# Performance work log

Hardware: AMD Instinct MI355X
Metric: run time of the kernel (lower is better)

## Reference

```python
import jax, jax.numpy as jnp
import numpy as np

N = 100_000       # nodes
E = 1_600_000     # directed edges (avg degree 16)
IN, H, Z = 128, 128, 64


def setup_inputs() -> dict:
    key = jax.random.key(0)
    ks = jax.random.split(key, 8)
    x = jax.random.normal(ks[0], (N, IN), dtype=jnp.float32)
    edge_index = jax.random.randint(ks[1], (2, E), 0, N, dtype=jnp.int32)
    # Glorot-ish init like PyG GCNConv
    W1 = jax.random.normal(ks[2], (IN, H), dtype=jnp.float32) / np.sqrt(IN).astype(np.float32)
    b1 = jnp.zeros((H,), dtype=jnp.float32)
    Wmu = jax.random.normal(ks[3], (H, Z), dtype=jnp.float32) / np.sqrt(H).astype(np.float32)
    bmu = jnp.zeros((Z,), dtype=jnp.float32)
    Wlv = jax.random.normal(ks[4], (H, Z), dtype=jnp.float32) / np.sqrt(H).astype(np.float32)
    blv = jnp.zeros((Z,), dtype=jnp.float32)
    return {"x": x, "edge_index": edge_index, "W1": W1, "b1": b1,
            "Wmu": Wmu, "bmu": bmu, "Wlv": Wlv, "blv": blv}


def _gcn_conv(x, src, dst, norm, W, b):
    """PyG GCNConv: out = scatter_add(norm * (x @ W)[src], dst) + b."""
    h = x @ W                                   # [N, out_dim]
    msg = h[src] * norm[:, None]                # [E+N, out_dim] gather + scale
    out = jax.ops.segment_sum(msg, dst, num_segments=N)
    return out + b


def reference(x, edge_index, W1, b1, Wmu, bmu, Wlv, blv):
    loop = jnp.arange(N, dtype=edge_index.dtype)
    src = jnp.concatenate([edge_index[0], loop])   # add self-loops (PyG default)
    dst = jnp.concatenate([edge_index[1], loop])
    # symmetric normalization D^{-1/2} (A+I) D^{-1/2}
    deg = jax.ops.segment_sum(jnp.ones_like(dst, dtype=x.dtype), dst, num_segments=N)
    dinv = jax.lax.rsqrt(deg)                      # deg >= 1 thanks to self-loops
    norm = dinv[src] * dinv[dst]                   # [E+N]
    h = jax.nn.relu(_gcn_conv(x, src, dst, norm, W1, b1))
    mu = _gcn_conv(h, src, dst, norm, Wmu, bmu)
    logvar = _gcn_conv(h, src, dst, norm, Wlv, blv)
    return (mu, logvar)
```

## Files before the change

### kernel.cpp

```cpp
#include <hip/hip_runtime.h>
#include <hip/hip_bf16.h>
#include <stdint.h>

static inline size_t ws_align(size_t x) { return (x + 255) & ~(size_t)255; }

typedef __attribute__((ext_vector_type(8))) short bf16x8;
typedef __attribute__((ext_vector_type(4))) float f32x4;

__device__ __forceinline__ uint32_t pack_bf16(float a, float b) {
    uint32_t ua = __float_as_uint(a), ub = __float_as_uint(b);
    ua = (ua + 0x7fffu + ((ua >> 16) & 1u)) >> 16;
    ub = (ub + 0x7fffu + ((ub >> 16) & 1u)) >> 16;
    return ua | (ub << 16);
}
__device__ __forceinline__ uint16_t cvt_bf16(float a) {
    uint32_t ua = __float_as_uint(a);
    return (uint16_t)((ua + 0x7fffu + ((ua >> 16) & 1u)) >> 16);
}
__device__ __forceinline__ float bf_lo(uint32_t v) { return __uint_as_float(v << 16); }
__device__ __forceinline__ float bf_hi(uint32_t v) { return __uint_as_float(v & 0xffff0000u); }


__global__ __launch_bounds__(256) void k_bcount(const int* __restrict__ dst, int* __restrict__ cntAB,
                                                int E, int nchunk, int NB) {
    __shared__ int h[512];
    for (int t = threadIdx.x; t < NB; t += 256) h[t] = 0;
    __syncthreads();
    const int c = blockIdx.x;
    const int per = (E + nchunk - 1) / nchunk;
    const int e0 = c * per, e1 = (e0 + per < E) ? e0 + per : E;
    for (int e = e0 + threadIdx.x; e < e1; e += 256)
        atomicAdd(&h[dst[e] >> 8], 1);
    __syncthreads();
    for (int t = threadIdx.x; t < NB; t += 256) cntAB[t * nchunk + c] = h[t];
}

__global__ __launch_bounds__(256) void k_bscatter(const int* __restrict__ src, const int* __restrict__ dst,
                                                  const int* __restrict__ baseAB, uint2* __restrict__ ebkt,
                                                  int E, int nchunk, int NB) {
    __shared__ int bump[512];
    const int c = blockIdx.x;
    for (int t = threadIdx.x; t < NB; t += 256) bump[t] = baseAB[t * nchunk + c];
    __syncthreads();
    const int per = (E + nchunk - 1) / nchunk;
    const int e0 = c * per, e1 = (e0 + per < E) ? e0 + per : E;
    for (int e = e0 + threadIdx.x; e < e1; e += 256) {
        int d = dst[e], s = src[e];
        int pos = atomicAdd(&bump[d >> 8], 1);
        ebkt[pos] = make_uint2((uint32_t)s, (uint32_t)d);
    }
}

__global__ __launch_bounds__(256) void k_bhist(const uint2* __restrict__ ebkt, const int* __restrict__ baseAB,
                                               int* __restrict__ cnt, float* __restrict__ dinv,
                                               int nchunk, int N) {
    __shared__ int h[256];
    h[threadIdx.x] = 0;
    __syncthreads();
    const int b = blockIdx.x;
    const int e0 = baseAB[b * nchunk], e1 = baseAB[(b + 1) * nchunk];
    for (int e = e0 + threadIdx.x; e < e1; e += 256)
        atomicAdd(&h[ebkt[e].y & 255], 1);
    __syncthreads();
    int node = (b << 8) + threadIdx.x;
    if (node < N) {
        int c = h[threadIdx.x];
        cnt[node] = c;
        dinv[node] = rsqrtf((float)(c + 1));
    }
}

__global__ __launch_bounds__(256) void k_bfill(const uint2* __restrict__ ebkt, const int* __restrict__ baseAB,
                                               const int* __restrict__ rp, const float* __restrict__ dinv,
                                               uint2* __restrict__ cedge, int nchunk) {
    __shared__ int fl[256];
    fl[threadIdx.x] = 0;
    __syncthreads();
    const int b = blockIdx.x;
    const int e0 = baseAB[b * nchunk], e1 = baseAB[(b + 1) * nchunk];
    for (int e = e0 + threadIdx.x; e < e1; e += 256) {
        uint2 sd = ebkt[e];
        int d = (int)sd.y;
        int posL = atomicAdd(&fl[d & 255], 1);
        cedge[rp[d] + posL] = make_uint2(sd.x, __float_as_uint(dinv[sd.x] * dinv[d]));
    }
}

__global__ __launch_bounds__(256) void k_scan1(const int* __restrict__ cnt, int* __restrict__ rp,
                                               int* __restrict__ bsum, int N) {
    __shared__ int sh[256];
    int t = threadIdx.x;
    int base = blockIdx.x * 1024 + t * 4;
    int v[4];
#pragma unroll
    for (int i = 0; i < 4; i++) v[i] = (base + i < N) ? cnt[base + i] : 0;
    int s = v[0] + v[1] + v[2] + v[3];
    sh[t] = s;
    __syncthreads();
    for (int off = 1; off < 256; off <<= 1) {
        int x = (t >= off) ? sh[t - off] : 0;
        __syncthreads();
        sh[t] += x;
        __syncthreads();
    }
    int excl = sh[t] - s;
    if (t == 255) bsum[blockIdx.x] = sh[255];
    int run = excl;
#pragma unroll
    for (int i = 0; i < 4; i++) {
        if (base + i < N) rp[base + i] = run;
        run += v[i];
    }
}

__global__ __launch_bounds__(256) void k_scan2(int* __restrict__ bsum, int nb) {
    __shared__ int sh[256];
    int t = threadIdx.x;
    int v = (t < nb) ? bsum[t] : 0;
    sh[t] = v;
    __syncthreads();
    for (int off = 1; off < 256; off <<= 1) {
        int x = (t >= off) ? sh[t - off] : 0;
        __syncthreads();
        sh[t] += x;
        __syncthreads();
    }
    if (t < nb) bsum[t] = sh[t] - v;
}

__global__ void k_scan3(int* __restrict__ rp, const int* __restrict__ bsum, int N, int E) {
    int i = blockIdx.x * blockDim.x + threadIdx.x;
    if (i < N) rp[i] += bsum[i >> 10];
    if (i == N) rp[N] = E;
}

__global__ void k_cvt(const float* __restrict__ in, uint32_t* __restrict__ outp, int n4) {
    int idx = blockIdx.x * blockDim.x + threadIdx.x;
    if (idx >= n4) return;
    float4 v = ((const float4*)in)[idx];
    ((uint2*)outp)[idx] = make_uint2(pack_bf16(v.x, v.y), pack_bf16(v.z, v.w));
}

__global__ __launch_bounds__(256) void k_agg(const uint8_t* __restrict__ featB,
                                             uint32_t* __restrict__ outB,
                                             const int* __restrict__ rp,
                                             const uint2* __restrict__ cedge,
                                             const float* __restrict__ dinv, int N) {
    int node = blockIdx.x * 4 + (threadIdx.x >> 6);
    if (node >= N) return;
    int lane = threadIdx.x & 63;
    int j = lane & 15;
    int q = lane >> 4;
    int beg = rp[node], end = rp[node + 1];
    float di = dinv[node];
    float w0 = (q == 0) ? di * di : 0.0f;

    uint4 sv = *(const uint4*)(featB + (size_t)node * 256 + j * 16);
    float acc[8];
    acc[0] = bf_lo(sv.x) * w0; acc[1] = bf_hi(sv.x) * w0;
    acc[2] = bf_lo(sv.y) * w0; acc[3] = bf_hi(sv.y) * w0;
    acc[4] = bf_lo(sv.z) * w0; acc[5] = bf_hi(sv.z) * w0;
    acc[6] = bf_lo(sv.w) * w0; acc[7] = bf_hi(sv.w) * w0;

    int i = beg + q;
    for (; i + 4 < end; i += 8) {
        uint2 ea = cedge[i], eb = cedge[i + 4];
        float wa = __uint_as_float(ea.y), wb = __uint_as_float(eb.y);
        uint4 ga = *(const uint4*)(featB + (size_t)ea.x * 256 + j * 16);
        uint4 gb = *(const uint4*)(featB + (size_t)eb.x * 256 + j * 16);
        acc[0] = fmaf(bf_lo(ga.x), wa, acc[0]); acc[1] = fmaf(bf_hi(ga.x), wa, acc[1]);
        acc[2] = fmaf(bf_lo(ga.y), wa, acc[2]); acc[3] = fmaf(bf_hi(ga.y), wa, acc[3]);
        acc[4] = fmaf(bf_lo(ga.z), wa, acc[4]); acc[5] = fmaf(bf_hi(ga.z), wa, acc[5]);
        acc[6] = fmaf(bf_lo(ga.w), wa, acc[6]); acc[7] = fmaf(bf_hi(ga.w), wa, acc[7]);
        acc[0] = fmaf(bf_lo(gb.x), wb, acc[0]); acc[1] = fmaf(bf_hi(gb.x), wb, acc[1]);
        acc[2] = fmaf(bf_lo(gb.y), wb, acc[2]); acc[3] = fmaf(bf_hi(gb.y), wb, acc[3]);
        acc[4] = fmaf(bf_lo(gb.z), wb, acc[4]); acc[5] = fmaf(bf_hi(gb.z), wb, acc[5]);
        acc[6] = fmaf(bf_lo(gb.w), wb, acc[6]); acc[7] = fmaf(bf_hi(gb.w), wb, acc[7]);
    }
    for (; i < end; i += 4) {
        uint2 ea = cedge[i];
        float wa = __uint_as_float(ea.y);
        uint4 ga = *(const uint4*)(featB + (size_t)ea.x * 256 + j * 16);
        acc[0] = fmaf(bf_lo(ga.x), wa, acc[0]); acc[1] = fmaf(bf_hi(ga.x), wa, acc[1]);
        acc[2] = fmaf(bf_lo(ga.y), wa, acc[2]); acc[3] = fmaf(bf_hi(ga.y), wa, acc[3]);
        acc[4] = fmaf(bf_lo(ga.z), wa, acc[4]); acc[5] = fmaf(bf_hi(ga.z), wa, acc[5]);
        acc[6] = fmaf(bf_lo(ga.w), wa, acc[6]); acc[7] = fmaf(bf_hi(ga.w), wa, acc[7]);
    }

#pragma unroll
    for (int k = 0; k < 8; k++) {
        acc[k] += __shfl_xor(acc[k], 16, 64);
        acc[k] += __shfl_xor(acc[k], 32, 64);
    }
    if (q == 0) {
        uint4 p = make_uint4(pack_bf16(acc[0], acc[1]), pack_bf16(acc[2], acc[3]),
                             pack_bf16(acc[4], acc[5]), pack_bf16(acc[6], acc[7]));
        *(uint4*)(outB + (size_t)node * 64 + j * 4) = p;
    }
}

__global__ __launch_bounds__(256) void k_gemm1_mfma(
        const uint8_t* __restrict__ A, uint8_t* __restrict__ C,
        const float* __restrict__ W, const float* __restrict__ bias, int N) {
    __shared__ uint32_t Bt[128 * 68];
    {
        int c = threadIdx.x & 127;
        for (int k2 = threadIdx.x >> 7; k2 < 64; k2 += 2)
            Bt[c * 68 + k2] = pack_bf16(W[(2 * k2) * 128 + c], W[(2 * k2 + 1) * 128 + c]);
    }
    __syncthreads();

    const int lane = threadIdx.x & 63;
    const int wv = threadIdx.x >> 6;
    const int rrow = lane & 15;
    const int g = lane >> 4;
    const int r0 = blockIdx.x * 64 + wv * 16;
    const int rl = r0 + rrow;
    const int rc = (rl < N) ? rl : (N - 1);

    bf16x8 a[4];
    const uint8_t* arow = A + (size_t)rc * 256 + g * 16;
#pragma unroll
    for (int kb = 0; kb < 4; kb++) a[kb] = *(const bf16x8*)(arow + kb * 64);

    f32x4 acc[8];
#pragma unroll
    for (int ct = 0; ct < 8; ct++) acc[ct] = (f32x4){0.f, 0.f, 0.f, 0.f};

    const char* btb = (const char*)Bt;
#pragma unroll
    for (int ct = 0; ct < 8; ct++) {
        const char* bp = btb + (ct * 16 + rrow) * 272 + g * 16;
#pragma unroll
        for (int kb = 0; kb < 4; kb++) {
            bf16x8 bfr = *(const bf16x8*)(bp + kb * 64);
            acc[ct] = __builtin_amdgcn_mfma_f32_16x16x32_bf16(a[kb], bfr, acc[ct], 0, 0, 0);
        }
    }

#pragma unroll
    for (int ct = 0; ct < 8; ct++) {
        const int col = ct * 16 + rrow;
        const float bv = bias[col];
#pragma unroll
        for (int r = 0; r < 4; r++) {
            int row = r0 + g * 4 + r;
            if (row < N) {
                float h = fmaxf(acc[ct][r] + bv, 0.f);
                *(uint16_t*)(C + (size_t)row * 256 + col * 2) = cvt_bf16(h);
            }
        }
    }
}

__global__ __launch_bounds__(256) void k_gemm2_mfma(
        const uint8_t* __restrict__ A, float* __restrict__ out,
        const float* __restrict__ Wmu, const float* __restrict__ Wlv,
        const float* __restrict__ bmu, const float* __restrict__ blv, int N) {
    __shared__ uint32_t Bt[128 * 68];
    {
        int c = threadIdx.x & 127;
        const float* Wc = (c < 64) ? (Wmu + c) : (Wlv + (c - 64));
        for (int k2 = threadIdx.x >> 7; k2 < 64; k2 += 2)
            Bt[c * 68 + k2] = pack_bf16(Wc[(2 * k2) * 64], Wc[(2 * k2 + 1) * 64]);
    }
    __syncthreads();

    const int lane = threadIdx.x & 63;
    const int wv = threadIdx.x >> 6;
    const int rrow = lane & 15;
    const int g = lane >> 4;
    const int r0 = blockIdx.x * 64 + wv * 16;
    const int rl = r0 + rrow;
    const int rc = (rl < N) ? rl : (N - 1);

    bf16x8 a[4];
    const uint8_t* arow = A + (size_t)rc * 256 + g * 16;
#pragma unroll
    for (int kb = 0; kb < 4; kb++) a[kb] = *(const bf16x8*)(arow + kb * 64);

    f32x4 acc[8];
#pragma unroll
    for (int ct = 0; ct < 8; ct++) acc[ct] = (f32x4){0.f, 0.f, 0.f, 0.f};

    const char* btb = (const char*)Bt;
#pragma unroll
    for (int ct = 0; ct < 8; ct++) {
        const char* bp = btb + (ct * 16 + rrow) * 272 + g * 16;
#pragma unroll
        for (int kb = 0; kb < 4; kb++) {
            bf16x8 bfr = *(const bf16x8*)(bp + kb * 64);
            acc[ct] = __builtin_amdgcn_mfma_f32_16x16x32_bf16(a[kb], bfr, acc[ct], 0, 0, 0);
        }
    }

#pragma unroll
    for (int ct = 0; ct < 8; ct++) {
        const int col = ct * 16 + rrow;
        const float bv = (col < 64) ? bmu[col] : blv[col - 64];
        float* obase = (col < 64) ? (out + col) : (out + (size_t)N * 64 + (col - 64));
#pragma unroll
        for (int r = 0; r < 4; r++) {
            int row = r0 + g * 4 + r;
            if (row < N) obase[(size_t)row * 64] = acc[ct][r] + bv;
        }
    }
}

extern "C" void kernel_launch(void* const* d_in, const int* in_sizes, int n_in,
                              void* d_out, int out_size, void* d_ws, size_t ws_size,
                              hipStream_t stream) {
    const float* x   = (const float*)d_in[0];
    const int*   ei  = (const int*)d_in[1];
    const float* W1  = (const float*)d_in[2];
    const float* b1  = (const float*)d_in[3];
    const float* Wmu = (const float*)d_in[4];
    const float* bmu = (const float*)d_in[5];
    const float* Wlv = (const float*)d_in[6];
    const float* blv = (const float*)d_in[7];
    float* out = (float*)d_out;

    const int N = in_sizes[0] / 128;
    const int E = in_sizes[1] / 2;
    const int* src = ei;
    const int* dst = ei + E;

    const int nchunk = 256;
    const int NB = (N + 255) >> 8;
    const int M = NB * nchunk;

    char* ws = (char*)d_ws;
    size_t off = 0;
    float* dinv   = (float*)(ws + off); off = ws_align(off + (size_t)N * 4);
    int* cnt      = (int*)(ws + off);   off = ws_align(off + (size_t)N * 4);
    int* rp       = (int*)(ws + off);   off = ws_align(off + (size_t)(N + 1) * 4);
    int* bsum     = (int*)(ws + off);   off = ws_align(off + 1024 * 4);
    int* cntAB    = (int*)(ws + off);   off = ws_align(off + (size_t)(M + 64) * 4);
    int* baseAB   = (int*)(ws + off);   off = ws_align(off + (size_t)(M + 64) * 4);
    uint2* cedge  = (uint2*)(ws + off); off = ws_align(off + (size_t)E * 8);
    uint32_t* xb  = (uint32_t*)(ws + off); off = ws_align(off + (size_t)N * 256);
    uint8_t* F1   = (uint8_t*)(ws + off);  off = ws_align(off + (size_t)N * 256);
    uint2* ebkt   = (uint2*)xb;

    const int b = 256;

    k_bcount<<<nchunk, 256, 0, stream>>>(dst, cntAB, E, nchunk, NB);
    k_scan1<<<(M + 1023) / 1024, 256, 0, stream>>>(cntAB, baseAB, bsum, M);
    k_scan2<<<1, 256, 0, stream>>>(bsum, (M + 1023) / 1024);
    k_scan3<<<(M + 1 + b - 1) / b, b, 0, stream>>>(baseAB, bsum, M, E);
    k_bscatter<<<nchunk, 256, 0, stream>>>(src, dst, baseAB, ebkt, E, nchunk, NB);
    k_bhist<<<NB, 256, 0, stream>>>(ebkt, baseAB, cnt, dinv, nchunk, N);
    k_scan1<<<(N + 1023) / 1024, 256, 0, stream>>>(cnt, rp, bsum, N);
    k_scan2<<<1, 256, 0, stream>>>(bsum, (N + 1023) / 1024);
    k_scan3<<<(N + 1 + b - 1) / b, b, 0, stream>>>(rp, bsum, N, E);
    k_bfill<<<NB, 256, 0, stream>>>(ebkt, baseAB, rp, dinv, cedge, nchunk);

    k_cvt<<<(N * 32 + b - 1) / b, b, 0, stream>>>(x, xb, N * 32);
    const int aggBlocks = (N + 3) / 4;
    k_agg<<<aggBlocks, 256, 0, stream>>>((const uint8_t*)xb, (uint32_t*)F1, rp, cedge, dinv, N);
    k_gemm1_mfma<<<(N + 63) / 64, 256, 0, stream>>>(F1, F1, W1, b1, N);

    k_agg<<<aggBlocks, 256, 0, stream>>>(F1, (uint32_t*)xb, rp, cedge, dinv, N);
    k_gemm2_mfma<<<(N + 63) / 64, 256, 0, stream>>>((const uint8_t*)xb, out, Wmu, Wlv, bmu, blv, N);
}
```

Baseline: 245.8 us.

## Fuse node rowptr scan into bucket histogram and unroll gather loop by four

```diff
diff --git a/kernel.cpp b/kernel.cpp
--- a/kernel.cpp
+++ b/kernel.cpp
@@ -19,6 +19,13 @@
 }
 __device__ __forceinline__ float bf_lo(uint32_t v) { return __uint_as_float(v << 16); }
 __device__ __forceinline__ float bf_hi(uint32_t v) { return __uint_as_float(v & 0xffff0000u); }
+
+__device__ __forceinline__ void fma8(float* acc, uint4 g, float wt) {
+    acc[0] = fmaf(bf_lo(g.x), wt, acc[0]); acc[1] = fmaf(bf_hi(g.x), wt, acc[1]);
+    acc[2] = fmaf(bf_lo(g.y), wt, acc[2]); acc[3] = fmaf(bf_hi(g.y), wt, acc[3]);
+    acc[4] = fmaf(bf_lo(g.z), wt, acc[4]); acc[5] = fmaf(bf_hi(g.z), wt, acc[5]);
+    acc[6] = fmaf(bf_lo(g.w), wt, acc[6]); acc[7] = fmaf(bf_hi(g.w), wt, acc[7]);
+}
 
 
 __global__ __launch_bounds__(256) void k_bcount(const int* __restrict__ dst, int* __restrict__ cntAB,
@@ -52,9 +59,10 @@
 }
 
 __global__ __launch_bounds__(256) void k_bhist(const uint2* __restrict__ ebkt, const int* __restrict__ baseAB,
-                                               int* __restrict__ cnt, float* __restrict__ dinv,
-                                               int nchunk, int N) {
+                                               float* __restrict__ dinv, int* __restrict__ rp,
+                                               int nchunk, int N, int E) {
     __shared__ int h[256];
+    __shared__ int sh[256];
     h[threadIdx.x] = 0;
     __syncthreads();
     const int b = blockIdx.x;
@@ -62,12 +70,22 @@
     for (int e = e0 + threadIdx.x; e < e1; e += 256)
         atomicAdd(&h[ebkt[e].y & 255], 1);
     __syncthreads();
-    int node = (b << 8) + threadIdx.x;
+    const int t = threadIdx.x;
+    const int c = h[t];
+    sh[t] = c;
+    __syncthreads();
+    for (int off = 1; off < 256; off <<= 1) {
+        int x = (t >= off) ? sh[t - off] : 0;
+        __syncthreads();
+        sh[t] += x;
+        __syncthreads();
+    }
+    int node = (b << 8) + t;
     if (node < N) {
-        int c = h[threadIdx.x];
-        cnt[node] = c;
+        rp[node] = e0 + sh[t] - c;
         dinv[node] = rsqrtf((float)(c + 1));
     }
+    if (blockIdx.x == gridDim.x - 1 && t == 0) rp[N] = E;
 }
 
 __global__ __launch_bounds__(256) void k_bfill(const uint2* __restrict__ ebkt, const int* __restrict__ baseAB,
@@ -154,37 +172,29 @@
     int beg = rp[node], end = rp[node + 1];
     float di = dinv[node];
     float w0 = (q == 0) ? di * di : 0.0f;
-
-    uint4 sv = *(const uint4*)(featB + (size_t)node * 256 + j * 16);
+    const uint8_t* fb = featB + (size_t)j * 16;
+
+    uint4 sv = *(const uint4*)(fb + (size_t)node * 256);
     float acc[8];
     acc[0] = bf_lo(sv.x) * w0; acc[1] = bf_hi(sv.x) * w0;
     acc[2] = bf_lo(sv.y) * w0; acc[3] = bf_hi(sv.y) * w0;
     acc[4] = bf_lo(sv.z) * w0; acc[5] = bf_hi(sv.z) * w0;
     acc[6] = bf_lo(sv.w) * w0; acc[7] = bf_hi(sv.w) * w0;
 
-    int i = beg + q;
-    for (; i + 4 < end; i += 8) {
-        uint2 ea = cedge[i], eb = cedge[i + 4];
-        float wa = __uint_as_float(ea.y), wb = __uint_as_float(eb.y);
-        uint4 ga = *(const uint4*)(featB + (size_t)ea.x * 256 + j * 16);
-        uint4 gb = *(const uint4*)(featB + (size_t)eb.x * 256 + j * 16);
-        acc[0] = fmaf(bf_lo(ga.x), wa, acc[0]); acc[1] = fmaf(bf_hi(ga.x), wa, acc[1]);
-        acc[2] = fmaf(bf_lo(ga.y), wa, acc[2]); acc[3] = fmaf(bf_hi(ga.y), wa, acc[3]);
-        acc[4] = fmaf(bf_lo(ga.z), wa, acc[4]); acc[5] = fmaf(bf_hi(ga.z), wa, acc[5]);
-        acc[6] = fmaf(bf_lo(ga.w), wa, acc[6]); acc[7] = fmaf(bf_hi(ga.w), wa, acc[7]);
-        acc[0] = fmaf(bf_lo(gb.x), wb, acc[0]); acc[1] = fmaf(bf_hi(gb.x), wb, acc[1]);
-        acc[2] = fmaf(bf_lo(gb.y), wb, acc[2]); acc[3] = fmaf(bf_hi(gb.y), wb, acc[3]);
-        acc[4] = fmaf(bf_lo(gb.z), wb, acc[4]); acc[5] = fmaf(bf_hi(gb.z), wb, acc[5]);
-        acc[6] = fmaf(bf_lo(gb.w), wb, acc[6]); acc[7] = fmaf(bf_hi(gb.w), wb, acc[7]);
-    }
-    for (; i < end; i += 4) {
-        uint2 ea = cedge[i];
-        float wa = __uint_as_float(ea.y);
-        uint4 ga = *(const uint4*)(featB + (size_t)ea.x * 256 + j * 16);
-        acc[0] = fmaf(bf_lo(ga.x), wa, acc[0]); acc[1] = fmaf(bf_hi(ga.x), wa, acc[1]);
-        acc[2] = fmaf(bf_lo(ga.y), wa, acc[2]); acc[3] = fmaf(bf_hi(ga.y), wa, acc[3]);
-        acc[4] = fmaf(bf_lo(ga.z), wa, acc[4]); acc[5] = fmaf(bf_hi(ga.z), wa, acc[5]);
-        acc[6] = fmaf(bf_lo(ga.w), wa, acc[6]); acc[7] = fmaf(bf_hi(ga.w), wa, acc[7]);
+    for (int base = beg + q; base < end; base += 16) {
+        uint2 e0 = cedge[base];
+        uint2 e1 = make_uint2(0u, 0u), e2 = make_uint2(0u, 0u), e3 = make_uint2(0u, 0u);
+        if (base + 4 < end)  e1 = cedge[base + 4];
+        if (base + 8 < end)  e2 = cedge[base + 8];
+        if (base + 12 < end) e3 = cedge[base + 12];
+        uint4 g0 = *(const uint4*)(fb + (size_t)e0.x * 256);
+        uint4 g1 = *(const uint4*)(fb + (size_t)e1.x * 256);
+        uint4 g2 = *(const uint4*)(fb + (size_t)e2.x * 256);
+        uint4 g3 = *(const uint4*)(fb + (size_t)e3.x * 256);
+        fma8(acc, g0, __uint_as_float(e0.y));
+        fma8(acc, g1, __uint_as_float(e1.y));
+        fma8(acc, g2, __uint_as_float(e2.y));
+        fma8(acc, g3, __uint_as_float(e3.y));
     }
 
 #pragma unroll
@@ -332,7 +342,6 @@
     char* ws = (char*)d_ws;
     size_t off = 0;
     float* dinv   = (float*)(ws + off); off = ws_align(off + (size_t)N * 4);
-    int* cnt      = (int*)(ws + off);   off = ws_align(off + (size_t)N * 4);
     int* rp       = (int*)(ws + off);   off = ws_align(off + (size_t)(N + 1) * 4);
     int* bsum     = (int*)(ws + off);   off = ws_align(off + 1024 * 4);
     int* cntAB    = (int*)(ws + off);   off = ws_align(off + (size_t)(M + 64) * 4);
@@ -349,10 +358,7 @@
     k_scan2<<<1, 256, 0, stream>>>(bsum, (M + 1023) / 1024);
     k_scan3<<<(M + 1 + b - 1) / b, b, 0, stream>>>(baseAB, bsum, M, E);
     k_bscatter<<<nchunk, 256, 0, stream>>>(src, dst, baseAB, ebkt, E, nchunk, NB);
-    k_bhist<<<NB, 256, 0, stream>>>(ebkt, baseAB, cnt, dinv, nchunk, N);
-    k_scan1<<<(N + 1023) / 1024, 256, 0, stream>>>(cnt, rp, bsum, N);
-    k_scan2<<<1, 256, 0, stream>>>(bsum, (N + 1023) / 1024);
-    k_scan3<<<(N + 1 + b - 1) / b, b, 0, stream>>>(rp, bsum, N, E);
+    k_bhist<<<NB, 256, 0, stream>>>(ebkt, baseAB, dinv, rp, nchunk, N, E);
     k_bfill<<<NB, 256, 0, stream>>>(ebkt, baseAB, rp, dinv, cedge, nchunk);
 
     k_cvt<<<(N * 32 + b - 1) / b, b, 0, stream>>>(x, xb, N * 32);
```

After: 240.2 us. 1.02x faster.
